# Optimization experiments

Hardware: AMD Instinct MI355X
Metric: run time of the kernel (lower is better)

Reference implementation:

```python
import jax, jax.numpy as jnp
import numpy as np

SIGMA = 10.0
# 24 neighbor offsets: all (dh, dw) in [-2,2]^2 except (0,0)
OFFSETS = [(dh, dw) for dh in range(-2, 3) for dw in range(-2, 3) if not (dh == 0 and dw == 0)]


def rgb2ycbcr(x):
    # x: [B,3,H,W]; flat @ mat + bias, exactly as the torch module (mat as written)
    mat = jnp.array([[0.257, -0.148, 0.439],
                     [0.564, -0.291, -0.368],
                     [0.098, 0.439, -0.071]], dtype=x.dtype)
    bias = jnp.array([16 / 255.0, 128 / 255.0, 128 / 255.0], dtype=x.dtype)
    # bchw -> bhwc contraction with mat, then back to bchw
    return jnp.einsum('bchw,ck->bkhw', x, mat) + bias[None, :, None, None]


def shifted_diff(a, dh, dw):
    # a[..., shifted slice] - a[..., opposite slice]; matches torch slicing exactly
    H, W = a.shape[-2], a.shape[-1]
    h1s, h1e = max(dh, 0), H + min(dh, 0)
    w1s, w1e = max(dw, 0), W + min(dw, 0)
    h2s, h2e = max(-dh, 0), H + min(-dh, 0)
    w2s, w2e = max(-dw, 0), W + min(-dw, 0)
    return a[..., h1s:h1e, w1s:w1e] - a[..., h2s:h2e, w2s:w2e]


def setup_inputs() -> dict:
    key = jax.random.key(0)
    k1, k2 = jax.random.split(key)
    B, C, H, W = 16, 3, 512, 512
    inp = jax.random.uniform(k1, (B, C, H, W), dtype=jnp.float32)
    out = jax.random.uniform(k2, (B, C, H, W), dtype=jnp.float32)
    return {"input": inp, "output": out}


def reference(input, output):
    x = rgb2ycbcr(input)
    y = output
    s = -1.0 / (2.0 * SIGMA * SIGMA)
    total = jnp.zeros((), dtype=x.dtype)
    for dh, dw in OFFSETS:
        dx = shifted_diff(x, dh, dw)
        dy = shifted_diff(y, dh, dw)
        w = jnp.exp(jnp.sum(dx * dx, axis=1, keepdims=True) * s)  # [B,1,h,w]
        l1 = jnp.sum(jnp.abs(dy), axis=1, keepdims=True)          # [B,1,h,w]
        total = total + jnp.mean(w * l1)
    return total / len(OFFSETS)
```

## Files before the change

### kernel.cpp

```cpp
#include <hip/hip_runtime.h>
#include <hip/hip_bf16.h>
#include <stdint.h>


#define B_ 16
#define H_ 512
#define W_ 512
#define HW_ (H_ * W_)
#define CHW_ (3 * HW_)

#define TH 4
#define ROWS 6
#define COLS 520
#define NTHREADS 512
#define POISON 1e19f
#define K2 0.08493218049364766f

__global__ void zero_out_kernel(float* p) { p[0] = 0.0f; }

__device__ __forceinline__ void gload16(const float* gsrc, float* ldst) {
  __builtin_amdgcn_global_load_lds(
      (const __attribute__((address_space(1))) void*)gsrc,
      (__attribute__((address_space(3))) void*)ldst, 16, 0, 0);
}

template <int DW>
__device__ __forceinline__ float contrib0(const float (&O)[6][8]) {
  const float scale = 2.0f / (24.0f * (float)B_ * (float)H_ * (float)(W_ - DW));
  float s = 0.0f;
#pragma unroll
  for (int p = 0; p < 4; ++p) {
    float d0 = O[0][p] - O[0][p + DW];
    float d1 = O[1][p] - O[1][p + DW];
    float d2 = O[2][p] - O[2][p + DW];
    float nq = -(d0 * d0 + d1 * d1 + d2 * d2);
    float wgt = __builtin_amdgcn_exp2f(nq);
    float l1 = fabsf(O[3][p] - O[3][p + DW]) + fabsf(O[4][p] - O[4][p + DW]) +
               fabsf(O[5][p] - O[5][p + DW]);
    s += wgt * l1;
  }
  return scale * s;
}

template <int DH, int DW>
__device__ __forceinline__ float contribN(const float (&O)[6][8],
                                          const float (&N)[6][12]) {
  constexpr int AW = DW < 0 ? -DW : DW;
  const float scale =
      2.0f / (24.0f * (float)B_ * (float)(H_ - DH) * (float)(W_ - AW));
  float s = 0.0f;
#pragma unroll
  for (int p = 0; p < 4; ++p) {
    const int ni = p + 4 + DW;
    float d0 = O[0][p] - N[0][ni];
    float d1 = O[1][p] - N[1][ni];
    float d2 = O[2][p] - N[2][ni];
    float nq = -(d0 * d0 + d1 * d1 + d2 * d2);
    float wgt = __builtin_amdgcn_exp2f(nq);
    float l1 = fabsf(O[3][p] - N[3][ni]) + fabsf(O[4][p] - N[4][ni]) +
               fabsf(O[5][p] - N[5][ni]);
    s += wgt * l1;
  }
  return scale * s;
}

__global__ __launch_bounds__(NTHREADS, 4) void smooth_loss_kernel(
    const float* __restrict__ in, const float* __restrict__ outp,
    float* __restrict__ result) {
  __shared__ alignas(16) float lds[6][ROWS][COLS];
  __shared__ float wsum[8];

  const int tid = threadIdx.x;
  const int wv = tid >> 6;
  const int lane = tid & 63;
  const int by = blockIdx.x;
  const int b = blockIdx.y;
  const int ibase = by * TH;

  const float* inb = in + (size_t)b * CHW_;
  const float* outb = outp + (size_t)b * CHW_;

#pragma unroll
  for (int k = 0; k < 9; ++k) {
    int wc = wv + 8 * k;
    int r = wc / 12;
    int rem = wc - 12 * r;
    int p = rem >> 1;
    int h = rem & 1;
    if (ibase + r < H_) {
      const float* src =
          (p < 3 ? inb + (size_t)p * HW_ : outb + (size_t)(p - 3) * HW_) +
          (size_t)(ibase + r) * W_ + 256 * h + 4 * lane;
      gload16(src, &lds[p][r][4 + 256 * h]);
    }
  }

  if (tid < 288) {
    int p = tid / 48;
    int rem = tid - 48 * p;
    int r = rem >> 3;
    int ci = rem & 7;
    int col = ci < 4 ? ci : 512 + ci;
    lds[p][r][col] = (p == 0) ? POISON : 0.0f;
  }
  if (ibase + TH >= H_) {
    for (int c = tid; c < 6 * 2 * COLS; c += NTHREADS) {
      int p = c / (2 * COLS);
      int rem = c - p * (2 * COLS);
      int r = 4 + rem / COLS;
      int col = rem % COLS;
      lds[p][r][col] = (p == 0) ? POISON : 0.0f;
    }
  }

  __syncthreads();

  {
#pragma unroll
    for (int k = 0; k < 2; ++k) {
      int c = tid + NTHREADS * k;
      if (c < ROWS * 130) {
        int r = c / 130;
        int q4 = c - 130 * r;
        int col = 4 * q4;
        float4 rr = *(const float4*)&lds[0][r][col];
        float4 gg = *(const float4*)&lds[1][r][col];
        float4 bb = *(const float4*)&lds[2][r][col];
        float rv[4] = {rr.x, rr.y, rr.z, rr.w};
        float gv[4] = {gg.x, gg.y, gg.z, gg.w};
        float bv[4] = {bb.x, bb.y, bb.z, bb.w};
        float x0[4], x1[4], x2[4];
#pragma unroll
        for (int m = 0; m < 4; ++m) {
          x0[m] = (0.257f * K2) * rv[m] + (0.564f * K2) * gv[m] + (0.098f * K2) * bv[m];
          x1[m] = (-0.148f * K2) * rv[m] + (-0.291f * K2) * gv[m] + (0.439f * K2) * bv[m];
          x2[m] = (0.439f * K2) * rv[m] + (-0.368f * K2) * gv[m] + (-0.071f * K2) * bv[m];
        }
        *(float4*)&lds[0][r][col] = make_float4(x0[0], x0[1], x0[2], x0[3]);
        *(float4*)&lds[1][r][col] = make_float4(x1[0], x1[1], x1[2], x1[3]);
        *(float4*)&lds[2][r][col] = make_float4(x2[0], x2[1], x2[2], x2[3]);
      }
    }
  }

  __syncthreads();

  const int half = wv >> 2;
  const int row = wv & 3;
  const int j0 = 256 * half + 4 * lane;

  float acc = 0.0f;
  float O[6][8];
#pragma unroll
  for (int p6 = 0; p6 < 6; ++p6) {
    *(float4*)&O[p6][0] = *(const float4*)&lds[p6][row][j0 + 4];
    *(float4*)&O[p6][4] = *(const float4*)&lds[p6][row][j0 + 8];
  }

  __builtin_amdgcn_s_setprio(1);
  acc += contrib0<1>(O);
  acc += contrib0<2>(O);
  __builtin_amdgcn_s_setprio(0);

  {
    float N[6][12];
#pragma unroll
    for (int p6 = 0; p6 < 6; ++p6) {
      *(float4*)&N[p6][0] = *(const float4*)&lds[p6][row + 1][j0];
      *(float4*)&N[p6][4] = *(const float4*)&lds[p6][row + 1][j0 + 4];
      *(float4*)&N[p6][8] = *(const float4*)&lds[p6][row + 1][j0 + 8];
    }
    __builtin_amdgcn_s_setprio(1);
    acc += contribN<1, -2>(O, N);
    acc += contribN<1, -1>(O, N);
    acc += contribN<1, 0>(O, N);
    acc += contribN<1, 1>(O, N);
    acc += contribN<1, 2>(O, N);
    __builtin_amdgcn_s_setprio(0);
  }
  {
    float N[6][12];
#pragma unroll
    for (int p6 = 0; p6 < 6; ++p6) {
      *(float4*)&N[p6][0] = *(const float4*)&lds[p6][row + 2][j0];
      *(float4*)&N[p6][4] = *(const float4*)&lds[p6][row + 2][j0 + 4];
      *(float4*)&N[p6][8] = *(const float4*)&lds[p6][row + 2][j0 + 8];
    }
    __builtin_amdgcn_s_setprio(1);
    acc += contribN<2, -2>(O, N);
    acc += contribN<2, -1>(O, N);
    acc += contribN<2, 0>(O, N);
    acc += contribN<2, 1>(O, N);
    acc += contribN<2, 2>(O, N);
    __builtin_amdgcn_s_setprio(0);
  }

#pragma unroll
  for (int o = 32; o > 0; o >>= 1) acc += __shfl_down(acc, o, 64);
  if (lane == 0) wsum[wv] = acc;
  __syncthreads();
  if (tid == 0) {
    float s = 0.0f;
#pragma unroll
    for (int wq = 0; wq < 8; ++wq) s += wsum[wq];
    atomicAdd(result, s);
  }
}

extern "C" void kernel_launch(void* const* d_in, const int* in_sizes, int n_in,
                              void* d_out, int out_size, void* d_ws, size_t ws_size,
                              hipStream_t stream) {
  const float* in = (const float*)d_in[0];
  const float* outp = (const float*)d_in[1];
  float* res = (float*)d_out;

  zero_out_kernel<<<1, 1, 0, stream>>>(res);

  dim3 grid(H_ / TH, B_, 1);
  smooth_loss_kernel<<<grid, NTHREADS, 0, stream>>>(in, outp, res);
}
```

Measured before the change: 49.52 us.

## Halve row tile to two rows with two pixels per thread

Shrinks each block's output tile from four rows to two. The block now loads four halo rows instead of six, and each thread handles two pixels instead of four, with wave segments over 128 columns. The LDS footprint and register use drop, so the launch bound is raised to allow six blocks per CU for better occupancy. In exchange, the halo rows overhead grows relative to useful rows (4 loaded per 2 computed vs 6 per 4), so global traffic per output rises, and twice as many blocks issue atomics.

```diff
diff --git a/kernel.cpp b/kernel.cpp
--- a/kernel.cpp
+++ b/kernel.cpp
@@ -9,8 +9,8 @@
 #define HW_ (H_ * W_)
 #define CHW_ (3 * HW_)
 
-#define TH 4
-#define ROWS 6
+#define TH 2
+#define ROWS 4
 #define COLS 520
 #define NTHREADS 512
 #define POISON 1e19f
@@ -25,11 +25,11 @@
 }
 
 template <int DW>
-__device__ __forceinline__ float contrib0(const float (&O)[6][8]) {
+__device__ __forceinline__ float contrib0(const float (&O)[6][4]) {
   const float scale = 2.0f / (24.0f * (float)B_ * (float)H_ * (float)(W_ - DW));
   float s = 0.0f;
 #pragma unroll
-  for (int p = 0; p < 4; ++p) {
+  for (int p = 0; p < 2; ++p) {
     float d0 = O[0][p] - O[0][p + DW];
     float d1 = O[1][p] - O[1][p + DW];
     float d2 = O[2][p] - O[2][p + DW];
@@ -43,15 +43,15 @@
 }
 
 template <int DH, int DW>
-__device__ __forceinline__ float contribN(const float (&O)[6][8],
-                                          const float (&N)[6][12]) {
+__device__ __forceinline__ float contribN(const float (&O)[6][4],
+                                          const float (&N)[6][6]) {
   constexpr int AW = DW < 0 ? -DW : DW;
   const float scale =
       2.0f / (24.0f * (float)B_ * (float)(H_ - DH) * (float)(W_ - AW));
   float s = 0.0f;
 #pragma unroll
-  for (int p = 0; p < 4; ++p) {
-    const int ni = p + 4 + DW;
+  for (int p = 0; p < 2; ++p) {
+    const int ni = p + 2 + DW;
     float d0 = O[0][p] - N[0][ni];
     float d1 = O[1][p] - N[1][ni];
     float d2 = O[2][p] - N[2][ni];
@@ -64,7 +64,7 @@
   return scale * s;
 }
 
-__global__ __launch_bounds__(NTHREADS, 4) void smooth_loss_kernel(
+__global__ __launch_bounds__(NTHREADS, 6) void smooth_loss_kernel(
     const float* __restrict__ in, const float* __restrict__ outp,
     float* __restrict__ result) {
   __shared__ alignas(16) float lds[6][ROWS][COLS];
@@ -81,7 +81,7 @@
   const float* outb = outp + (size_t)b * CHW_;
 
 #pragma unroll
-  for (int k = 0; k < 9; ++k) {
+  for (int k = 0; k < 6; ++k) {
     int wc = wv + 8 * k;
     int r = wc / 12;
     int rem = wc - 12 * r;
@@ -95,21 +95,22 @@
     }
   }
 
-  if (tid < 288) {
-    int p = tid / 48;
-    int rem = tid - 48 * p;
+  if (tid < 192) {
+    int p = tid / 32;
+    int rem = tid - 32 * p;
     int r = rem >> 3;
     int ci = rem & 7;
     int col = ci < 4 ? ci : 512 + ci;
     lds[p][r][col] = (p == 0) ? POISON : 0.0f;
   }
-  if (ibase + TH >= H_) {
-    for (int c = tid; c < 6 * 2 * COLS; c += NTHREADS) {
-      int p = c / (2 * COLS);
-      int rem = c - p * (2 * COLS);
-      int r = 4 + rem / COLS;
-      int col = rem % COLS;
-      lds[p][r][col] = (p == 0) ? POISON : 0.0f;
+  if (ibase + 2 >= H_) {
+    for (int c = tid; c < 6 * 2 * 130; c += NTHREADS) {
+      int p = c / 260;
+      int rem = c - 260 * p;
+      int r = 2 + rem / 130;
+      int q4 = rem % 130;
+      float v = (p == 0) ? POISON : 0.0f;
+      *(float4*)&lds[p][r][4 * q4] = make_float4(v, v, v, v);
     }
   }
 
@@ -145,16 +146,16 @@
 
   __syncthreads();
 
-  const int half = wv >> 2;
-  const int row = wv & 3;
-  const int j0 = 256 * half + 4 * lane;
+  const int row = wv & 1;
+  const int seg = wv >> 1;
+  const int lc = 128 * seg + 2 * lane + 4;
 
   float acc = 0.0f;
-  float O[6][8];
+  float O[6][4];
 #pragma unroll
   for (int p6 = 0; p6 < 6; ++p6) {
-    *(float4*)&O[p6][0] = *(const float4*)&lds[p6][row][j0 + 4];
-    *(float4*)&O[p6][4] = *(const float4*)&lds[p6][row][j0 + 8];
+    *(float2*)&O[p6][0] = *(const float2*)&lds[p6][row][lc];
+    *(float2*)&O[p6][2] = *(const float2*)&lds[p6][row][lc + 2];
   }
 
   __builtin_amdgcn_s_setprio(1);
@@ -163,12 +164,12 @@
   __builtin_amdgcn_s_setprio(0);
 
   {
-    float N[6][12];
+    float N[6][6];
 #pragma unroll
     for (int p6 = 0; p6 < 6; ++p6) {
-      *(float4*)&N[p6][0] = *(const float4*)&lds[p6][row + 1][j0];
-      *(float4*)&N[p6][4] = *(const float4*)&lds[p6][row + 1][j0 + 4];
-      *(float4*)&N[p6][8] = *(const float4*)&lds[p6][row + 1][j0 + 8];
+      *(float2*)&N[p6][0] = *(const float2*)&lds[p6][row + 1][lc - 2];
+      *(float2*)&N[p6][2] = *(const float2*)&lds[p6][row + 1][lc];
+      *(float2*)&N[p6][4] = *(const float2*)&lds[p6][row + 1][lc + 2];
     }
     __builtin_amdgcn_s_setprio(1);
     acc += contribN<1, -2>(O, N);
@@ -179,12 +180,12 @@
     __builtin_amdgcn_s_setprio(0);
   }
   {
-    float N[6][12];
+    float N[6][6];
 #pragma unroll
     for (int p6 = 0; p6 < 6; ++p6) {
-      *(float4*)&N[p6][0] = *(const float4*)&lds[p6][row + 2][j0];
-      *(float4*)&N[p6][4] = *(const float4*)&lds[p6][row + 2][j0 + 4];
-      *(float4*)&N[p6][8] = *(const float4*)&lds[p6][row + 2][j0 + 8];
+      *(float2*)&N[p6][0] = *(const float2*)&lds[p6][row + 2][lc - 2];
+      *(float2*)&N[p6][2] = *(const float2*)&lds[p6][row + 2][lc];
+      *(float2*)&N[p6][4] = *(const float2*)&lds[p6][row + 2][lc + 2];
     }
     __builtin_amdgcn_s_setprio(1);
     acc += contribN<2, -2>(O, N);
```

New measurement: 74.94 us. 1.51x slower.
